# Kernel tuning notes

Hardware: AMD Instinct MI355X
Metric: run time of the kernel (lower is better)

The kernel has to match this reference:

```python
import jax, jax.numpy as jnp
import numpy as np

B, N, C_IN, C_OUT = 128, 512, 64, 64
ALPHA = 0.2  # LeakyReLU negative slope
NEG_INF = -9e15


def setup_inputs() -> dict:
    key = jax.random.key(0)
    k_x, k_adj, k_W, k_a, k_b = jax.random.split(key, 5)
    x = jax.random.normal(k_x, (B, N, C_IN), dtype=jnp.float32)
    adj = jax.random.randint(k_adj, (N, N), 0, 2, dtype=jnp.int32)
    # Xavier-uniform-ish init for W:[2,C_IN,C_OUT] and a:[2*C_OUT,1]
    limW = 1.414 * np.sqrt(6.0 / (C_IN + C_OUT))
    W = jax.random.uniform(k_W, (2, C_IN, C_OUT), jnp.float32, -limW, limW)
    lima = 1.414 * np.sqrt(6.0 / (2 * C_OUT + 1))
    a = jax.random.uniform(k_a, (2 * C_OUT, 1), jnp.float32, -lima, lima)
    stdv = 1.0 / np.sqrt(C_OUT)
    bias = jax.random.uniform(k_b, (C_OUT,), jnp.float32, -stdv, stdv)
    return {"x": x, "adj": adj, "W": W, "a": a, "bias": bias}


def reference(x, adj, W, a, bias):
    F_out = W.shape[2]
    h0 = jnp.einsum('bnc,cf->bnf', x, W[0])
    h1 = jnp.einsum('bnc,cf->bnf', x, W[1])
    h = h0 + h1  # [B,N,F]
    # Separable additive attention score: e[b,i,j] = leaky(a1.h_i + a2.h_j)
    a1 = a[:F_out, 0]
    a2 = a[F_out:, 0]
    s1 = h @ a1  # [B,N]
    s2 = h @ a2  # [B,N]
    e = jax.nn.leaky_relu(s1[:, :, None] + s2[:, None, :], negative_slope=ALPHA)
    att = jnp.where(adj[None, :, :] > 0, e, NEG_INF)
    att = jax.nn.softmax(att, axis=2)  # [B,N,N]
    # attention*M (M=eye) picks diagonal -> route through h0; off-diagonal -> h1
    eye = jnp.eye(att.shape[1], dtype=att.dtype)
    diag = jnp.einsum('bii->bi', att)
    h_prime = diag[:, :, None] * h0 + jnp.einsum('bij,bjf->bif', att * (1.0 - eye), h1)
    return h_prime + bias
```

## Files before the change

### kernel.cpp

```cpp
#include <hip/hip_runtime.h>
#include <hip/hip_bf16.h>

#define BB 128
#define NN 512
#define ALPHA_ 0.2f
#define NEG_INF_ -9.0e15f
#define SPB 536
#define SXW 72

typedef short bf16x8 __attribute__((ext_vector_type(8)));
typedef short bf16x4 __attribute__((ext_vector_type(4)));
typedef float f32x4  __attribute__((ext_vector_type(4)));

__device__ __forceinline__ float bf2f(__hip_bfloat16 v) { return __bfloat162float(v); }
__device__ __forceinline__ float bfs2f(short s) {
    unsigned u = ((unsigned)(unsigned short)s) << 16;
    return __uint_as_float(u);
}

__global__ __launch_bounds__(256, 2) void k1_proj(
    const float* __restrict__ x, const float* __restrict__ W, const float* __restrict__ a,
    const int* __restrict__ adj, unsigned char* __restrict__ bits,
    __hip_bfloat16* __restrict__ h1T, __hip_bfloat16* __restrict__ h0T,
    float* __restrict__ s1, float* __restrict__ s2)
{
    if (blockIdx.x >= 1024) {
        int idx = (blockIdx.x - 1024) * 256 + threadIdx.x;
        const int* p = adj + (size_t)idx * 8;
        unsigned m = 0;
        #pragma unroll
        for (int t = 0; t < 8; ++t) m |= (p[t] > 0 ? 1u : 0u) << t;
        bits[idx] = (unsigned char)m;
        return;
    }

    __shared__ __align__(16) unsigned short sX[64 * SXW];
    __shared__ __align__(16) unsigned short sWb[2][64 * SXW];
    __shared__ unsigned short sT[64 * 66];
    int tid = threadIdx.x, lane = tid & 63, w = tid >> 6;
    int lane15 = lane & 15, quad = lane >> 4;
    int b = blockIdx.x >> 3, n0 = (blockIdx.x & 7) << 6;

    for (int idx = tid; idx < 4096; idx += 256) {
        int c = idx >> 6, f = idx & 63;
        __hip_bfloat16 b0 = __float2bfloat16(W[idx]);
        __hip_bfloat16 b1 = __float2bfloat16(W[4096 + idx]);
        sWb[0][f * SXW + c] = *(unsigned short*)&b0;
        sWb[1][f * SXW + c] = *(unsigned short*)&b1;
    }
    {
        int nl = tid >> 2, q = tid & 3;
        const float* xp = x + ((size_t)b * NN + n0 + nl) * 64 + q * 16;
        float4 v0 = *(const float4*)(xp + 0);
        float4 v1 = *(const float4*)(xp + 4);
        float4 v2 = *(const float4*)(xp + 8);
        float4 v3 = *(const float4*)(xp + 12);
        union { bf16x8 v; __hip_bfloat16 h[8]; } pk0, pk1;
        pk0.h[0]=__float2bfloat16(v0.x); pk0.h[1]=__float2bfloat16(v0.y);
        pk0.h[2]=__float2bfloat16(v0.z); pk0.h[3]=__float2bfloat16(v0.w);
        pk0.h[4]=__float2bfloat16(v1.x); pk0.h[5]=__float2bfloat16(v1.y);
        pk0.h[6]=__float2bfloat16(v1.z); pk0.h[7]=__float2bfloat16(v1.w);
        pk1.h[0]=__float2bfloat16(v2.x); pk1.h[1]=__float2bfloat16(v2.y);
        pk1.h[2]=__float2bfloat16(v2.z); pk1.h[3]=__float2bfloat16(v2.w);
        pk1.h[4]=__float2bfloat16(v3.x); pk1.h[5]=__float2bfloat16(v3.y);
        pk1.h[6]=__float2bfloat16(v3.z); pk1.h[7]=__float2bfloat16(v3.w);
        *(bf16x8*)&sX[nl * SXW + q * 16]     = pk0.v;
        *(bf16x8*)&sX[nl * SXW + q * 16 + 8] = pk1.v;
    }
    __syncthreads();

    f32x4 acc0[4] = {{0,0,0,0},{0,0,0,0},{0,0,0,0},{0,0,0,0}};
    f32x4 acc1[4] = {{0,0,0,0},{0,0,0,0},{0,0,0,0},{0,0,0,0}};
    #pragma unroll
    for (int kt = 0; kt < 2; ++kt) {
        bf16x8 af = *(const bf16x8*)&sX[(w * 16 + lane15) * SXW + kt * 32 + quad * 8];
        #pragma unroll
        for (int nt = 0; nt < 4; ++nt) {
            bf16x8 b0 = *(const bf16x8*)&sWb[0][(nt * 16 + lane15) * SXW + kt * 32 + quad * 8];
            acc0[nt] = __builtin_amdgcn_mfma_f32_16x16x32_bf16(af, b0, acc0[nt], 0, 0, 0);
            bf16x8 b1 = *(const bf16x8*)&sWb[1][(nt * 16 + lane15) * SXW + kt * 32 + quad * 8];
            acc1[nt] = __builtin_amdgcn_mfma_f32_16x16x32_bf16(af, b1, acc1[nt], 0, 0, 0);
        }
    }

    float a1v[4], a2v[4];
    #pragma unroll
    for (int nt = 0; nt < 4; ++nt) {
        a1v[nt] = a[nt * 16 + lane15];
        a2v[nt] = a[64 + nt * 16 + lane15];
    }
    float p1[4] = {0, 0, 0, 0}, p2[4] = {0, 0, 0, 0};
    #pragma unroll
    for (int nt = 0; nt < 4; ++nt) {
        #pragma unroll
        for (int r = 0; r < 4; ++r) {
            int nl = w * 16 + quad * 4 + r;
            int f  = nt * 16 + lane15;
            float h0v = acc0[nt][r], h1v = acc1[nt][r];
            __hip_bfloat16 hb = __float2bfloat16(h1v);
            sT[f * 66 + nl] = *(unsigned short*)&hb;
            float hs = h0v + h1v;
            p1[r] = fmaf(hs, a1v[nt], p1[r]);
            p2[r] = fmaf(hs, a2v[nt], p2[r]);
        }
    }
    #pragma unroll
    for (int r = 0; r < 4; ++r) {
        float v1 = p1[r], v2 = p2[r];
        #pragma unroll
        for (int o = 1; o < 16; o <<= 1) {
            v1 += __shfl_xor(v1, o, 64);
            v2 += __shfl_xor(v2, o, 64);
        }
        if (lane15 == 0) {
            int row = b * NN + n0 + w * 16 + quad * 4 + r;
            s1[row] = v1; s2[row] = v2;
        }
    }
    __syncthreads();
    unsigned short* h1Tu = (unsigned short*)h1T;
    #pragma unroll
    for (int fr = 0; fr < 16; ++fr) {
        int f = w * 16 + fr;
        h1Tu[(size_t)b * 32768 + f * 512 + n0 + lane] = sT[f * 66 + lane];
    }
    __syncthreads();
    #pragma unroll
    for (int nt = 0; nt < 4; ++nt) {
        #pragma unroll
        for (int r = 0; r < 4; ++r) {
            int nl = w * 16 + quad * 4 + r;
            int f  = nt * 16 + lane15;
            __hip_bfloat16 hb = __float2bfloat16(acc0[nt][r]);
            sT[f * 66 + nl] = *(unsigned short*)&hb;
        }
    }
    __syncthreads();
    unsigned short* h0Tu = (unsigned short*)h0T;
    #pragma unroll
    for (int fr = 0; fr < 16; ++fr) {
        int f = w * 16 + fr;
        h0Tu[(size_t)b * 32768 + f * 512 + n0 + lane] = sT[f * 66 + lane];
    }
}

__global__ __launch_bounds__(256, 2) void k2_att(
    const unsigned char* __restrict__ adjbits,
    const float* __restrict__ bias,
    const __hip_bfloat16* __restrict__ h1T,
    const __hip_bfloat16* __restrict__ h0T,
    const float* __restrict__ s1, const float* __restrict__ s2,
    float* __restrict__ out)
{
    __shared__ __align__(16) __hip_bfloat16 sPb[32 * SPB];
    __shared__ float sInv[32], sPi[32];
    int tid = threadIdx.x, w = tid >> 6, lane = tid & 63;
    int b = blockIdx.y, i0 = blockIdx.x * 32;

    const float* s2b = s2 + (size_t)b * NN;
    float4 q0 = *(const float4*)(s2b + lane * 8);
    float4 q1 = *(const float4*)(s2b + lane * 8 + 4);
    float sv[8] = {q0.x, q0.y, q0.z, q0.w, q1.x, q1.y, q1.z, q1.w};

    const float* s1p = s1 + (size_t)b * NN + i0 + 8 * w;
    float4 sA = *(const float4*)(s1p + 0);
    float4 sB = *(const float4*)(s1p + 4);
    float s1r[8] = {sA.x, sA.y, sA.z, sA.w, sB.x, sB.y, sB.z, sB.w};

    #pragma unroll
    for (int r2 = 0; r2 < 8; ++r2) {
        int r = 8 * w + r2;
        int i = i0 + r;
        float s1i = s1r[r2];
        unsigned mb = adjbits[(size_t)i * 64 + lane];
        float p[8], ls = 0.f;
        #pragma unroll
        for (int t = 0; t < 8; ++t) {
            float s = s1i + sv[t];
            s = fmaxf(s, ALPHA_ * s);
            float e = (mb & (1u << t)) ? s : NEG_INF_;
            p[t] = __expf(e);
            ls += p[t];
        }
        #pragma unroll
        for (int o = 32; o > 0; o >>= 1) ls += __shfl_xor(ls, o, 64);
        if (lane == 0) sInv[r] = 1.f / ls;
        if ((i >> 3) == lane) {
            sPi[r] = p[i & 7];
            p[i & 7] = 0.f;
        }
        union { bf16x8 v; __hip_bfloat16 h[8]; } pk;
        #pragma unroll
        for (int t = 0; t < 8; ++t) pk.h[t] = __float2bfloat16(p[t]);
        *(bf16x8*)&sPb[r * SPB + lane * 8] = pk.v;
    }
    __syncthreads();

    int lane15 = lane & 15, quad = lane >> 4;
    int n0w = w * 16;
    const __hip_bfloat16* h1b = h1T + (size_t)b * 32768;
    const __hip_bfloat16* bptr = h1b + (size_t)(n0w + lane15) * 512 + quad * 8;
    const __hip_bfloat16* aptr0 = &sPb[lane15 * SPB + quad * 8];
    const __hip_bfloat16* aptr1 = &sPb[(16 + lane15) * SPB + quad * 8];
    f32x4 acc0 = {0, 0, 0, 0}, acc1 = {0, 0, 0, 0};
    bf16x8 bfr[8];
    #pragma unroll
    for (int half = 0; half < 2; ++half) {
        #pragma unroll
        for (int g = 0; g < 8; ++g)
            bfr[g] = *(const bf16x8*)(bptr + (half * 8 + g) * 32);
        #pragma unroll
        for (int g = 0; g < 8; ++g) {
            int kt = half * 8 + g;
            bf16x8 a0 = *(const bf16x8*)(aptr0 + kt * 32);
            acc0 = __builtin_amdgcn_mfma_f32_16x16x32_bf16(a0, bfr[g], acc0, 0, 0, 0);
            bf16x8 a1 = *(const bf16x8*)(aptr1 + kt * 32);
            acc1 = __builtin_amdgcn_mfma_f32_16x16x32_bf16(a1, bfr[g], acc1, 0, 0, 0);
        }
    }

    int f = n0w + lane15;
    float biasf = bias[f];
    const unsigned short* h0row = (const unsigned short*)h0T + (size_t)b * 32768 + (size_t)f * 512;
    #pragma unroll
    for (int t = 0; t < 2; ++t) {
        f32x4 ac = t ? acc1 : acc0;
        bf16x4 hv4 = *(const bf16x4*)(h0row + i0 + t * 16 + quad * 4);
        #pragma unroll
        for (int r = 0; r < 4; ++r) {
            int m = t * 16 + quad * 4 + r;
            int i = i0 + m;
            float h0v = bfs2f(hv4[r]);
            float inv = sInv[m], pi = sPi[m];
            out[((size_t)b * NN + i) * 64 + f] = ac[r] * inv + pi * inv * h0v + biasf;
        }
    }
}

extern "C" void kernel_launch(void* const* d_in, const int* in_sizes, int n_in,
                              void* d_out, int out_size, void* d_ws, size_t ws_size,
                              hipStream_t stream) {
    const void* p_x = nullptr; const void* p_adj = nullptr; const void* p_W = nullptr;
    const void* p_a = nullptr; const void* p_bias = nullptr;
    for (int k = 0; k < n_in; ++k) {
        switch (in_sizes[k]) {
            case 128 * 512 * 64: p_x    = d_in[k]; break;
            case 512 * 512:      p_adj  = d_in[k]; break;
            case 2 * 64 * 64:    p_W    = d_in[k]; break;
            case 2 * 64:         p_a    = d_in[k]; break;
            case 64:             p_bias = d_in[k]; break;
        }
    }
    const float* x    = (const float*)p_x;
    const int*   adj  = (const int*)p_adj;
    const float* W    = (const float*)p_W;
    const float* a    = (const float*)p_a;
    const float* bias = (const float*)p_bias;
    float* out = (float*)d_out;

    __hip_bfloat16* h1T = (__hip_bfloat16*)d_ws;
    __hip_bfloat16* h0T = h1T + 4194304;
    float* s1 = (float*)(h0T + 4194304);
    float* s2 = s1 + 65536;
    unsigned char* adjbits = (unsigned char*)(s2 + 65536);

    k1_proj<<<dim3(BB * 8 + 128), 256, 0, stream>>>(x, W, a, adj, adjbits, h1T, h0T, s1, s2);
    k2_att<<<dim3(NN / 32, BB), 256, 0, stream>>>(adjbits, bias, h1T, h0T, s1, s2, out);
}
```

Measured before the change: 108.6 us.

## Fold diagonal term via h0-h1 correction and drop transposed h0 pass

The diagonal probability is no longer zeroed out of the P matrix. The P@h1 product now includes the diagonal, and a correction pi*(h0-h1) is added in the epilogue. The projection kernel writes g=h0-h1 directly in row-major form, which removes the second LDS transpose pass with its two barriers. Other changes: launch bounds raised to 4 blocks per CU, a 1D grid swizzle for k2 work ordering, and the g loads hoisted before the MFMA loop. Risks are extra bf16 rounding from using the rounded diagonal value, and strided 2-byte global stores for g.

```diff
diff --git a/kernel.cpp b/kernel.cpp
--- a/kernel.cpp
+++ b/kernel.cpp
@@ -9,19 +9,17 @@
 #define SXW 72
 
 typedef short bf16x8 __attribute__((ext_vector_type(8)));
-typedef short bf16x4 __attribute__((ext_vector_type(4)));
 typedef float f32x4  __attribute__((ext_vector_type(4)));
 
-__device__ __forceinline__ float bf2f(__hip_bfloat16 v) { return __bfloat162float(v); }
-__device__ __forceinline__ float bfs2f(short s) {
-    unsigned u = ((unsigned)(unsigned short)s) << 16;
+__device__ __forceinline__ float bfs2f(unsigned short s) {
+    unsigned u = ((unsigned)s) << 16;
     return __uint_as_float(u);
 }
 
-__global__ __launch_bounds__(256, 2) void k1_proj(
+__global__ __launch_bounds__(256, 4) void k1_proj(
     const float* __restrict__ x, const float* __restrict__ W, const float* __restrict__ a,
     const int* __restrict__ adj, unsigned char* __restrict__ bits,
-    __hip_bfloat16* __restrict__ h1T, __hip_bfloat16* __restrict__ h0T,
+    __hip_bfloat16* __restrict__ h1T, __hip_bfloat16* __restrict__ gN,
     float* __restrict__ s1, float* __restrict__ s2)
 {
     if (blockIdx.x >= 1024) {
@@ -90,6 +88,7 @@
         a2v[nt] = a[64 + nt * 16 + lane15];
     }
     float p1[4] = {0, 0, 0, 0}, p2[4] = {0, 0, 0, 0};
+    unsigned short* gNu = (unsigned short*)gN + (size_t)b * 32768 + (size_t)n0 * 64;
     #pragma unroll
     for (int nt = 0; nt < 4; ++nt) {
         #pragma unroll
@@ -99,6 +98,8 @@
             float h0v = acc0[nt][r], h1v = acc1[nt][r];
             __hip_bfloat16 hb = __float2bfloat16(h1v);
             sT[f * 66 + nl] = *(unsigned short*)&hb;
+            __hip_bfloat16 gb16 = __float2bfloat16(h0v - h1v);
+            gNu[(size_t)nl * 64 + f] = *(unsigned short*)&gb16;
             float hs = h0v + h1v;
             p1[r] = fmaf(hs, a1v[nt], p1[r]);
             p2[r] = fmaf(hs, a2v[nt], p2[r]);
@@ -124,38 +125,23 @@
         int f = w * 16 + fr;
         h1Tu[(size_t)b * 32768 + f * 512 + n0 + lane] = sT[f * 66 + lane];
     }
-    __syncthreads();
-    #pragma unroll
-    for (int nt = 0; nt < 4; ++nt) {
-        #pragma unroll
-        for (int r = 0; r < 4; ++r) {
-            int nl = w * 16 + quad * 4 + r;
-            int f  = nt * 16 + lane15;
-            __hip_bfloat16 hb = __float2bfloat16(acc0[nt][r]);
-            sT[f * 66 + nl] = *(unsigned short*)&hb;
-        }
-    }
-    __syncthreads();
-    unsigned short* h0Tu = (unsigned short*)h0T;
-    #pragma unroll
-    for (int fr = 0; fr < 16; ++fr) {
-        int f = w * 16 + fr;
-        h0Tu[(size_t)b * 32768 + f * 512 + n0 + lane] = sT[f * 66 + lane];
-    }
-}
-
-__global__ __launch_bounds__(256, 2) void k2_att(
+}
+
+__global__ __launch_bounds__(256, 4) void k2_att(
     const unsigned char* __restrict__ adjbits,
     const float* __restrict__ bias,
     const __hip_bfloat16* __restrict__ h1T,
-    const __hip_bfloat16* __restrict__ h0T,
+    const __hip_bfloat16* __restrict__ gN,
     const float* __restrict__ s1, const float* __restrict__ s2,
     float* __restrict__ out)
 {
     __shared__ __align__(16) __hip_bfloat16 sPb[32 * SPB];
     __shared__ float sInv[32], sPi[32];
     int tid = threadIdx.x, w = tid >> 6, lane = tid & 63;
-    int b = blockIdx.y, i0 = blockIdx.x * 32;
+    int F = blockIdx.x;
+    int work = (F & 7) * 256 + (F >> 3);
+    int b = work >> 4;
+    int i0 = (work & 15) << 5;
 
     const float* s2b = s2 + (size_t)b * NN;
     float4 q0 = *(const float4*)(s2b + lane * 8);
@@ -185,23 +171,32 @@
         #pragma unroll
         for (int o = 32; o > 0; o >>= 1) ls += __shfl_xor(ls, o, 64);
         if (lane == 0) sInv[r] = 1.f / ls;
-        if ((i >> 3) == lane) {
-            sPi[r] = p[i & 7];
-            p[i & 7] = 0.f;
-        }
         union { bf16x8 v; __hip_bfloat16 h[8]; } pk;
         #pragma unroll
         for (int t = 0; t < 8; ++t) pk.h[t] = __float2bfloat16(p[t]);
+        if (lane == (i >> 3)) sPi[r] = __bfloat162float(pk.h[r2]);
         *(bf16x8*)&sPb[r * SPB + lane * 8] = pk.v;
     }
     __syncthreads();
 
     int lane15 = lane & 15, quad = lane >> 4;
     int n0w = w * 16;
+    int f = n0w + lane15;
+    float biasf = bias[f];
     const __hip_bfloat16* h1b = h1T + (size_t)b * 32768;
     const __hip_bfloat16* bptr = h1b + (size_t)(n0w + lane15) * 512 + quad * 8;
     const __hip_bfloat16* aptr0 = &sPb[lane15 * SPB + quad * 8];
     const __hip_bfloat16* aptr1 = &sPb[(16 + lane15) * SPB + quad * 8];
+
+    const unsigned short* gb = (const unsigned short*)gN + (size_t)b * 32768 + f;
+    unsigned short gvw[8];
+    #pragma unroll
+    for (int t = 0; t < 2; ++t) {
+        #pragma unroll
+        for (int r = 0; r < 4; ++r)
+            gvw[t * 4 + r] = gb[(size_t)(i0 + t * 16 + quad * 4 + r) * 64];
+    }
+
     f32x4 acc0 = {0, 0, 0, 0}, acc1 = {0, 0, 0, 0};
     bf16x8 bfr[8];
     #pragma unroll
@@ -219,20 +214,16 @@
         }
     }
 
-    int f = n0w + lane15;
-    float biasf = bias[f];
-    const unsigned short* h0row = (const unsigned short*)h0T + (size_t)b * 32768 + (size_t)f * 512;
     #pragma unroll
     for (int t = 0; t < 2; ++t) {
         f32x4 ac = t ? acc1 : acc0;
-        bf16x4 hv4 = *(const bf16x4*)(h0row + i0 + t * 16 + quad * 4);
         #pragma unroll
         for (int r = 0; r < 4; ++r) {
             int m = t * 16 + quad * 4 + r;
             int i = i0 + m;
-            float h0v = bfs2f(hv4[r]);
+            float gv = bfs2f(gvw[t * 4 + r]);
             float inv = sInv[m], pi = sPi[m];
-            out[((size_t)b * NN + i) * 64 + f] = ac[r] * inv + pi * inv * h0v + biasf;
+            out[((size_t)b * NN + i) * 64 + f] = (ac[r] + pi * gv) * inv + biasf;
         }
     }
 }
@@ -259,11 +250,11 @@
     float* out = (float*)d_out;
 
     __hip_bfloat16* h1T = (__hip_bfloat16*)d_ws;
-    __hip_bfloat16* h0T = h1T + 4194304;
-    float* s1 = (float*)(h0T + 4194304);
+    __hip_bfloat16* gN  = h1T + 4194304;
+    float* s1 = (float*)(gN + 4194304);
     float* s2 = s1 + 65536;
     unsigned char* adjbits = (unsigned char*)(s2 + 65536);
 
-    k1_proj<<<dim3(BB * 8 + 128), 256, 0, stream>>>(x, W, a, adj, adjbits, h1T, h0T, s1, s2);
-    k2_att<<<dim3(NN / 32, BB), 256, 0, stream>>>(adjbits, bias, h1T, h0T, s1, s2, out);
-}
+    k1_proj<<<dim3(BB * 8 + 128), 256, 0, stream>>>(x, W, a, adj, adjbits, h1T, gN, s1, s2);
+    k2_att<<<dim3(BB * NN / 32), 256, 0, stream>>>(adjbits, bias, h1T, gN, s1, s2, out);
+}
```

Result: no change. 106.6 us (-1.8%).
